# Kernel optimization log

Hardware: AMD Instinct MI355X
Metric: run time of the kernel (lower is better)

## Reference

```python
import jax, jax.numpy as jnp
import numpy as np

EPS = 1e-6
NUM_HEADS = 8
ATTN_DIM = 64
LINEAR_DIM = 64


def _layer_norm(x, eps=EPS):
    # F.layer_norm without elementwise affine
    mu = jnp.mean(x, axis=-1, keepdims=True)
    var = jnp.mean(jnp.square(x - mu), axis=-1, keepdims=True)
    return (x - mu) * jax.lax.rsqrt(var + eps)


def setup_inputs() -> dict:
    key = jax.random.key(0)
    k1, k2, k3 = jax.random.split(key, 3)
    B, N, D = 4, 2048, 512
    x = jax.random.normal(k1, (B, N, D), dtype=jnp.float32)
    invalid_attn_mask = jnp.tril(jnp.ones((N, N), dtype=jnp.float32))  # causal
    uvqk = jax.random.normal(k2, (D, 2 * LINEAR_DIM * NUM_HEADS + 2 * ATTN_DIM * NUM_HEADS), dtype=jnp.float32) * 0.02
    o_w = jax.random.normal(k3, (D, LINEAR_DIM * NUM_HEADS), dtype=jnp.float32) * (1.0 / np.sqrt(D))  # torch Linear weight [out, in]
    o_b = jnp.zeros((D,), dtype=jnp.float32)
    return {"x": x, "invalid_attn_mask": invalid_attn_mask, "uvqk": uvqk, "o_w": o_w, "o_b": o_b}


def reference(x, invalid_attn_mask, uvqk, o_w, o_b):
    B, N, D = x.shape
    H, dA, dL = NUM_HEADS, ATTN_DIM, LINEAR_DIM
    normed_x = _layer_norm(x)
    # fused uvqk projection + silu activation
    proj = jax.nn.silu(jnp.einsum('bnd,de->bne', normed_x, uvqk))
    u, v, q, k = jnp.split(proj, [dL * H, 2 * dL * H, 2 * dL * H + dA * H], axis=-1)
    q_h = q.reshape(B, N, H, dA)
    k_h = k.reshape(B, N, H, dA)
    v_h = v.reshape(B, N, H, dL)
    # HSTU attention: SiLU(qk)/N, then mask multiply (no softmax)
    qk_attn = jnp.einsum('bnhd,bmhd->bhnm', q_h, k_h)
    qk_attn = jax.nn.silu(qk_attn) / N
    qk_attn = qk_attn * invalid_attn_mask[None, None, :, :]
    attn = jnp.einsum('bhnm,bmhd->bnhd', qk_attn, v_h).reshape(B, N, H * dL)
    a = _layer_norm(attn)
    o_input = u * a
    out = jnp.einsum('bnf,df->bnd', o_input, o_w) + o_b + x
    return out
```

## Files before the change

kernel.cpp:

```cpp
#include <hip/hip_runtime.h>
#include <cstdint>

#define NTOK 2048
#define DIM 512
#define EDIM 2048
#define BATCH 4
#define HEADS 8
#define BNROWS 8192
#define INV_N (1.0f/2048.0f)

typedef unsigned short u16;
typedef __bf16 bf16x8 __attribute__((ext_vector_type(8)));
typedef u16   u16x8  __attribute__((ext_vector_type(8)));
typedef u16   u16x4  __attribute__((ext_vector_type(4)));
typedef float f32x4  __attribute__((ext_vector_type(4)));

__device__ __forceinline__ u16 f2bf(float f) {
  union { float f; uint32_t u; } v; v.f = f;
  uint32_t r = v.u + 0x7FFFu + ((v.u >> 16) & 1u);
  return (u16)(r >> 16);
}
__device__ __forceinline__ u16 f2bfc(float f) {
  return __builtin_bit_cast(u16, (__bf16)f);
}
__device__ __forceinline__ float bf2f(u16 b) {
  union { uint32_t u; float f; } v; v.u = ((uint32_t)b) << 16;
  return v.f;
}
__device__ __forceinline__ bf16x8 ldb(const u16* p) {
  u16x8 r = *(const u16x8*)p;
  return __builtin_bit_cast(bf16x8, r);
}
#define MFMA16(a,b,c) __builtin_amdgcn_mfma_f32_16x16x32_bf16((a),(b),(c),0,0,0)

__device__ __forceinline__ float silu_nr(float s) {
  float e = __expf(-s);
  e = fminf(e, 1.7e38f);
  float d = 1.0f + e;
  float r = __builtin_amdgcn_rcpf(d);
  r = r * fmaf(-d, r, 2.0f);
  return s * r;
}

__device__ __forceinline__ void gload16(const u16* g, u16* lds) {
  __builtin_amdgcn_global_load_lds(
      (const __attribute__((address_space(1))) void*)g,
      (__attribute__((address_space(3))) void*)lds, 16, 0, 0);
}

__global__ __launch_bounds__(256) void k_pre(const float* __restrict__ uvqk,
                                             const float* __restrict__ ow,
                                             const float* __restrict__ x,
                                             u16* __restrict__ uvqk_t,
                                             u16* __restrict__ ow_bf,
                                             u16* __restrict__ xn) {
  __shared__ float tile[32][33];
  int bid = blockIdx.x, tid = threadIdx.x;
  if (bid < 1024) {
    int tx = tid & 31, ty = tid >> 5;
    int j0 = (bid & 63) * 32, k0 = (bid >> 6) * 32;
#pragma unroll
    for (int r = ty; r < 32; r += 8)
      tile[r][tx] = uvqk[(size_t)(k0 + r) * EDIM + j0 + tx];
    __syncthreads();
#pragma unroll
    for (int r = ty; r < 32; r += 8)
      uvqk_t[(size_t)(j0 + r) * DIM + k0 + tx] = f2bfc(tile[tx][r]);
  } else if (bid < 1280) {
    int i4 = (bid - 1024) * 1024 + tid * 4;
    float4 v = *(const float4*)(ow + i4);
    u16x4 o = {f2bfc(v.x), f2bfc(v.y), f2bfc(v.z), f2bfc(v.w)};
    *(u16x4*)(ow_bf + i4) = o;
  } else {
    int lane = tid & 63, wid = tid >> 6;
    size_t row = (size_t)(bid - 1280) * 4 + wid;
    const float* xr = x + row * DIM;
    float4 a = ((const float4*)xr)[lane * 2];
    float4 b = ((const float4*)xr)[lane * 2 + 1];
    float s = a.x + a.y + a.z + a.w + b.x + b.y + b.z + b.w;
#pragma unroll
    for (int o = 32; o; o >>= 1) s += __shfl_xor(s, o);
    float mu = s * (1.0f / DIM);
    float d[8] = {a.x - mu, a.y - mu, a.z - mu, a.w - mu,
                  b.x - mu, b.y - mu, b.z - mu, b.w - mu};
    float v = 0.f;
#pragma unroll
    for (int j = 0; j < 8; ++j) v += d[j] * d[j];
#pragma unroll
    for (int o = 32; o; o >>= 1) v += __shfl_xor(v, o);
    float rs = rsqrtf(v * (1.0f / DIM) + 1e-6f);
    u16x8 o8;
#pragma unroll
    for (int j = 0; j < 8; ++j) o8[j] = f2bfc(d[j] * rs);
    *(u16x8*)(xn + row * DIM + lane * 8) = o8;
  }
}

__global__ __launch_bounds__(256, 2) void k_gemm1(const u16* __restrict__ A,
                                                  const u16* __restrict__ Bt,
                                                  u16* __restrict__ P,
                                                  u16* __restrict__ vt) {
  __shared__ u16 As[128 * 64];
  __shared__ u16 Bs[256 * 64];
  int tid = threadIdx.x, lane = tid & 63, wid = tid >> 6;
  int lm = lane & 15, lg = lane >> 4;
  int wr = wid >> 1, wc = wid & 1;

  int bid = blockIdx.x;
  int xcd = bid & 7, idx = bid >> 3;
  int r0 = (xcd * 8 + (idx >> 3)) * 128;
  int c0 = (idx & 7) * 256;

  int srow = tid >> 3;
  int scol = ((lane & 7) ^ (lane >> 3)) * 8;

  f32x4 acc[4][8];
  f32x4 z = {0.f, 0.f, 0.f, 0.f};
#pragma unroll
  for (int mt = 0; mt < 4; ++mt)
#pragma unroll
    for (int nt = 0; nt < 8; ++nt) acc[mt][nt] = z;

  int ksw = (lm & 7) << 3;

  for (int ks = 0; ks < DIM / 64; ++ks) {
#pragma unroll
    for (int it = 0; it < 4; ++it)
      gload16(A + (size_t)(r0 + it * 32 + srow) * DIM + ks * 64 + scol,
              As + it * 2048 + wid * 512);
#pragma unroll
    for (int it = 0; it < 8; ++it)
      gload16(Bt + (size_t)(c0 + it * 32 + srow) * DIM + ks * 64 + scol,
              Bs + it * 2048 + wid * 512);
    __syncthreads();

#pragma unroll
    for (int kk = 0; kk < 2; ++kk) {
      bf16x8 am[4], bn[8];
#pragma unroll
      for (int mt = 0; mt < 4; ++mt)
        am[mt] = ldb(&As[(wr * 64 + mt * 16 + lm) * 64 + ((kk * 32 + lg * 8) ^ ksw)]);
#pragma unroll
      for (int nt = 0; nt < 8; ++nt)
        bn[nt] = ldb(&Bs[(wc * 128 + nt * 16 + lm) * 64 + ((kk * 32 + lg * 8) ^ ksw)]);
#pragma unroll
      for (int mt = 0; mt < 4; ++mt)
#pragma unroll
        for (int nt = 0; nt < 8; ++nt)
          acc[mt][nt] = MFMA16(am[mt], bn[nt], acc[mt][nt]);
    }
    __syncthreads();
  }

  bool isv = (c0 >= 512) && (c0 < 1024);
  int btc = r0 >> 11;
  int nbw = (r0 & 2047) + wr * 64;
  int cw = c0 + wc * 128;

#pragma unroll
  for (int mt = 0; mt < 4; ++mt)
#pragma unroll
    for (int nt = 0; nt < 8; ++nt) {
      u16 pv[4];
#pragma unroll
      for (int i = 0; i < 4; ++i)
        pv[i] = f2bfc(silu_nr(acc[mt][nt][i]));
      if (isv) {
        int hv = (cw + nt * 16 - 512) >> 6;
        int e = (nt & 3) * 16 + lm;
        int n = nbw + mt * 16 + lg * 4;
        u16x4 pk = {pv[0], pv[1], pv[2], pv[3]};
        *(u16x4*)(vt + ((size_t)(btc * 8 + hv) * 64 + e) * NTOK + n) = pk;
      } else {
        int col = cw + nt * 16 + lm;
#pragma unroll
        for (int i = 0; i < 4; ++i) {
          size_t row = r0 + wr * 64 + mt * 16 + lg * 4 + i;
          P[row * EDIM + col] = pv[i];
        }
      }
    }
}

__global__ __launch_bounds__(256) void k_attn(const u16* __restrict__ proj,
                                              const u16* __restrict__ vt,
                                              u16* __restrict__ attnb) {
  __shared__ u16 kv0[8192];
  __shared__ u16 kv1[8192];
  __shared__ u16 p_lds[4][16][64];
  int tid = threadIdx.x, lane = tid & 63, w = tid >> 6;
  int lm = lane & 15, lg = lane >> 4;

  int bid = blockIdx.x;
  int xcd = bid & 7, idx = bid >> 3;
  int j = idx >> 2, pj = j & 7;
  int qtile = (j < 8) ? (31 - pj) : (j < 16) ? (16 + pj)
                      : (j < 24) ? (15 - pj) : pj;
  int bh = (xcd << 2) + (idx & 3);
  int b = bh >> 3, h = bh & 7;
  int n0 = qtile * 64;
  int nrow = n0 + w * 16;
  int nlm = nrow + lm;

  const u16* pb = proj + (size_t)b * NTOK * EDIM;
  const u16* kb = pb + 1536 + h * 64;
  const u16* vb = vt + (size_t)bh * 64 * NTOK;

  f32x4 z = {0.f, 0.f, 0.f, 0.f};

  int sr = lane >> 3;
  int sc = ((lane & 7) ^ sr) * 8;
  const u16* ks0 = kb + (size_t)(w * 16 + sr) * EDIM + sc;
  const u16* ks1 = kb + (size_t)(w * 16 + 8 + sr) * EDIM + sc;
  const u16* vs0 = vb + (size_t)(w * 16 + sr) * NTOK + sc;
  const u16* vs1 = vb + (size_t)(w * 16 + 8 + sr) * NTOK + sc;

  const u16* qrow = pb + (size_t)nlm * EDIM + 1024 + h * 64 + lg * 8;
  bf16x8 qf0 = ldb(qrow), qf1 = ldb(qrow + 32);

  f32x4 acc[4];
#pragma unroll
  for (int et = 0; et < 4; ++et) acc[et] = z;

  int psw = (lm & 7) << 3;

  gload16(ks0, kv0 + (w * 16) * 64);
  gload16(ks1, kv0 + (w * 16 + 8) * 64);
  gload16(vs0, kv0 + 4096 + (w * 16) * 64);
  gload16(vs1, kv0 + 4096 + (w * 16 + 8) * 64);
  asm volatile("s_waitcnt vmcnt(0)" ::: "memory");
  __builtin_amdgcn_s_barrier();

  int ntl = qtile + 1;
  for (int t = 0; t < ntl; ++t) {
    const u16* kt = (t & 1) ? kv1 : kv0;
    const u16* vl = kt + 4096;
    if (t + 1 < ntl) {
      u16* kd = ((t + 1) & 1) ? kv1 : kv0;
      size_t ko = (size_t)(t + 1) * 64 * EDIM;
      size_t vo = (size_t)(t + 1) * 64;
      gload16(ks0 + ko, kd + (w * 16) * 64);
      gload16(ks1 + ko, kd + (w * 16 + 8) * 64);
      gload16(vs0 + vo, kd + 4096 + (w * 16) * 64);
      gload16(vs1 + vo, kd + 4096 + (w * 16 + 8) * 64);
    }
    bf16x8 kf[4][2];
#pragma unroll
    for (int mb = 0; mb < 4; ++mb)
#pragma unroll
      for (int kk = 0; kk < 2; ++kk)
        kf[mb][kk] = ldb(&kt[(mb * 16 + lm) * 64 +
                             ((kk * 32 + lg * 8) ^ ((lm & 7) << 3))]);
    if (t == qtile) {
#pragma unroll
      for (int mb = 0; mb < 4; ++mb) {
        f32x4 s = MFMA16(kf[mb][0], qf0, z);
        s = MFMA16(kf[mb][1], qf1, s);
        int m = t * 64 + mb * 16 + lg * 4;
        u16x4 pk;
#pragma unroll
        for (int i = 0; i < 4; ++i)
          pk[i] = (m + i <= nlm) ? f2bfc(silu_nr(s[i])) : (u16)0;
        *(u16x4*)&p_lds[w][lm][(mb * 16 + lg * 4) ^ psw] = pk;
      }
    } else {
#pragma unroll
      for (int mb = 0; mb < 4; ++mb) {
        f32x4 s = MFMA16(kf[mb][0], qf0, z);
        s = MFMA16(kf[mb][1], qf1, s);
        u16x4 pk;
#pragma unroll
        for (int i = 0; i < 4; ++i) pk[i] = f2bfc(silu_nr(s[i]));
        *(u16x4*)&p_lds[w][lm][(mb * 16 + lg * 4) ^ psw] = pk;
      }
    }
    bf16x8 vf[2][4];
#pragma unroll
    for (int kk = 0; kk < 2; ++kk)
#pragma unroll
      for (int et = 0; et < 4; ++et)
        vf[kk][et] = ldb(&vl[(et * 16 + lm) * 64 +
                             ((kk * 32 + lg * 8) ^ ((lm & 7) << 3))]);
    bf16x8 pf0 = ldb(&p_lds[w][lm][(lg * 8) ^ psw]);
    bf16x8 pf1 = ldb(&p_lds[w][lm][(32 + lg * 8) ^ psw]);
#pragma unroll
    for (int et = 0; et < 4; ++et) {
      acc[et] = MFMA16(pf0, vf[0][et], acc[et]);
      acc[et] = MFMA16(pf1, vf[1][et], acc[et]);
    }
    asm volatile("s_waitcnt vmcnt(0)" ::: "memory");
    __builtin_amdgcn_s_barrier();
  }

#pragma unroll
  for (int et = 0; et < 4; ++et)
#pragma unroll
    for (int i = 0; i < 4; ++i)
      attnb[((size_t)b * NTOK + nrow + lg * 4 + i) * DIM +
            h * 64 + et * 16 + lm] = f2bfc(acc[et][i] * INV_N);
}

__global__ __launch_bounds__(256) void k_gemm2f(const u16* __restrict__ attnb,
                                                const u16* __restrict__ proj,
                                                const u16* __restrict__ Bw,
                                                const float* __restrict__ o_b,
                                                const float* __restrict__ x,
                                                float* __restrict__ out) {
  __shared__ u16 os[32 * 512];
  int tid = threadIdx.x, lane = tid & 63, w = tid >> 6;
  int lm = lane & 15, lg = lane >> 4;

  int bid = blockIdx.x;
  int xcd = bid & 7, idx = bid >> 3;
  int r0 = (xcd * 32 + idx) * 32;

#pragma unroll
  for (int rr = 0; rr < 8; ++rr) {
    int r = w * 8 + rr;
    u16x8 a8 = *(const u16x8*)(attnb + (size_t)(r0 + r) * DIM + lane * 8);
    float av[8];
#pragma unroll
    for (int j = 0; j < 8; ++j) av[j] = bf2f(a8[j]);
    float s = av[0] + av[1] + av[2] + av[3] + av[4] + av[5] + av[6] + av[7];
#pragma unroll
    for (int o = 32; o; o >>= 1) s += __shfl_xor(s, o);
    float mu = s * (1.0f / DIM);
    float d[8];
#pragma unroll
    for (int j = 0; j < 8; ++j) d[j] = av[j] - mu;
    float v = 0.f;
#pragma unroll
    for (int j = 0; j < 8; ++j) v += d[j] * d[j];
#pragma unroll
    for (int o = 32; o; o >>= 1) v += __shfl_xor(v, o);
    float rs = rsqrtf(v * (1.0f / DIM) + 1e-6f);
    u16x8 u8 = *(const u16x8*)(proj + (size_t)(r0 + r) * EDIM + lane * 8);
    u16x8 o8;
#pragma unroll
    for (int j = 0; j < 8; ++j) o8[j] = f2bfc(bf2f(u8[j]) * (d[j] * rs));
    *(u16x8*)&os[r * 512 + ((lane * 8) ^ ((r & 7) << 3))] = o8;
  }
  __syncthreads();

  int cb = w * 128;
  f32x4 acc[2][8];
  f32x4 z = {0.f, 0.f, 0.f, 0.f};
#pragma unroll
  for (int mt = 0; mt < 2; ++mt)
#pragma unroll
    for (int nt = 0; nt < 8; ++nt) acc[mt][nt] = z;

#pragma unroll 2
  for (int kc = 0; kc < 16; ++kc) {
    bf16x8 af[2];
#pragma unroll
    for (int mt = 0; mt < 2; ++mt)
      af[mt] = ldb(&os[(mt * 16 + lm) * 512 +
                       ((kc * 32 + lg * 8) ^ ((lm & 7) << 3))]);
    bf16x8 bfr[8];
#pragma unroll
    for (int nt = 0; nt < 8; ++nt)
      bfr[nt] = ldb(Bw + (size_t)(cb + nt * 16 + lm) * DIM + kc * 32 + lg * 8);
#pragma unroll
    for (int mt = 0; mt < 2; ++mt)
#pragma unroll
      for (int nt = 0; nt < 8; ++nt)
        acc[mt][nt] = MFMA16(af[mt], bfr[nt], acc[mt][nt]);
  }

#pragma unroll
  for (int mt = 0; mt < 2; ++mt)
#pragma unroll
    for (int nt = 0; nt < 8; ++nt)
#pragma unroll
      for (int i = 0; i < 4; ++i) {
        size_t row = r0 + mt * 16 + lg * 4 + i;
        int col = cb + nt * 16 + lm;
        out[row * DIM + col] = acc[mt][nt][i] + o_b[col] + x[row * DIM + col];
      }
}

extern "C" void kernel_launch(void* const* d_in, const int* in_sizes, int n_in,
                              void* d_out, int out_size, void* d_ws, size_t ws_size,
                              hipStream_t stream) {
  const float* x    = (const float*)d_in[0];
  const float* uvqk = (const float*)d_in[2];
  const float* o_w  = (const float*)d_in[3];
  const float* o_b  = (const float*)d_in[4];
  float* out = (float*)d_out;

  u16* uvqk_t = (u16*)d_ws;
  u16* ow_bf  = uvqk_t + (size_t)EDIM * DIM;
  u16* xn     = ow_bf + (size_t)DIM * DIM;
  u16* proj   = xn + (size_t)BNROWS * DIM;
  u16* attnb  = proj + (size_t)BNROWS * EDIM;
  u16* vt     = attnb + (size_t)BNROWS * DIM;

  k_pre<<<dim3(3328), 256, 0, stream>>>(uvqk, o_w, x, uvqk_t, ow_bf, xn);
  k_gemm1<<<dim3(512), 256, 0, stream>>>(xn, uvqk_t, proj, vt);
  k_attn<<<dim3(1024), 256, 0, stream>>>(proj, vt, attnb);
  k_gemm2f<<<dim3(256), 256, 0, stream>>>(attnb, proj, ow_bf, o_b, x, out);
}
```

Baseline: 97.37 us.

## Software-pipeline gemm1 K loop with double-buffered A and register-staged B

Restructures the uvqk projection GEMM main loop so the next K slice is fetched while the current one is computed. A is double-buffered in LDS via direct global-to-LDS loads, and B is prefetched into registers and written to a single LDS buffer after a barrier. This is meant to hide global memory latency behind MFMA work, at the cost of more LDS, extra registers for the B staging (which may hurt occupancy at 2 blocks per CU), and an additional barrier per iteration.

```diff
diff --git a/kernel.cpp b/kernel.cpp
--- a/kernel.cpp
+++ b/kernel.cpp
@@ -100,7 +100,7 @@
                                                   const u16* __restrict__ Bt,
                                                   u16* __restrict__ P,
                                                   u16* __restrict__ vt) {
-  __shared__ u16 As[128 * 64];
+  __shared__ u16 As[2][128 * 64];
   __shared__ u16 Bs[256 * 64];
   int tid = threadIdx.x, lane = tid & 63, wid = tid >> 6;
   int lm = lane & 15, lg = lane >> 4;
@@ -113,6 +113,7 @@
 
   int srow = tid >> 3;
   int scol = ((lane & 7) ^ (lane >> 3)) * 8;
+  int ldsb = wid * 512 + (lane & 63) * 8;
 
   f32x4 acc[4][8];
   f32x4 z = {0.f, 0.f, 0.f, 0.f};
@@ -123,23 +124,38 @@
 
   int ksw = (lm & 7) << 3;
 
+#pragma unroll
+  for (int it = 0; it < 4; ++it)
+    gload16(A + (size_t)(r0 + it * 32 + srow) * DIM + scol,
+            As[0] + it * 2048 + wid * 512);
+#pragma unroll
+  for (int it = 0; it < 8; ++it)
+    gload16(Bt + (size_t)(c0 + it * 32 + srow) * DIM + scol,
+            Bs + it * 2048 + wid * 512);
+  asm volatile("s_waitcnt vmcnt(0)" ::: "memory");
+  __builtin_amdgcn_s_barrier();
+
+  int cur = 0;
   for (int ks = 0; ks < DIM / 64; ++ks) {
-#pragma unroll
-    for (int it = 0; it < 4; ++it)
-      gload16(A + (size_t)(r0 + it * 32 + srow) * DIM + ks * 64 + scol,
-              As + it * 2048 + wid * 512);
-#pragma unroll
-    for (int it = 0; it < 8; ++it)
-      gload16(Bt + (size_t)(c0 + it * 32 + srow) * DIM + ks * 64 + scol,
-              Bs + it * 2048 + wid * 512);
-    __syncthreads();
+    u16x8 rb[8];
+    bool pre = (ks + 1 < DIM / 64);
+    if (pre) {
+#pragma unroll
+      for (int it = 0; it < 4; ++it)
+        gload16(A + (size_t)(r0 + it * 32 + srow) * DIM + (ks + 1) * 64 + scol,
+                As[cur ^ 1] + it * 2048 + wid * 512);
+#pragma unroll
+      for (int it = 0; it < 8; ++it)
+        rb[it] = *(const u16x8*)(Bt + (size_t)(c0 + it * 32 + srow) * DIM +
+                                 (ks + 1) * 64 + scol);
+    }
 
 #pragma unroll
     for (int kk = 0; kk < 2; ++kk) {
       bf16x8 am[4], bn[8];
 #pragma unroll
       for (int mt = 0; mt < 4; ++mt)
-        am[mt] = ldb(&As[(wr * 64 + mt * 16 + lm) * 64 + ((kk * 32 + lg * 8) ^ ksw)]);
+        am[mt] = ldb(&As[cur][(wr * 64 + mt * 16 + lm) * 64 + ((kk * 32 + lg * 8) ^ ksw)]);
 #pragma unroll
       for (int nt = 0; nt < 8; ++nt)
         bn[nt] = ldb(&Bs[(wc * 128 + nt * 16 + lm) * 64 + ((kk * 32 + lg * 8) ^ ksw)]);
@@ -149,7 +165,15 @@
         for (int nt = 0; nt < 8; ++nt)
           acc[mt][nt] = MFMA16(am[mt], bn[nt], acc[mt][nt]);
     }
+
+    __builtin_amdgcn_s_barrier();
+    if (pre) {
+#pragma unroll
+      for (int it = 0; it < 8; ++it)
+        *(u16x8*)(Bs + it * 2048 + ldsb) = rb[it];
+    }
     __syncthreads();
+    cur ^= 1;
   }
 
   bool isv = (c0 >= 512) && (c0 < 1024);
```

Result: no change. 97.47 us (+0.1%).
